# Kernel tuning notes

Hardware: AMD Instinct MI355X
Metric: run time of the kernel (lower is better)

The kernel has to match this reference:

```python
import jax, jax.numpy as jnp
import numpy as np

TAU_MEM = 10.0
TAU_SYN = 5.0
REFRACTORY = 2.0
THRESHOLD = 1.0
TRACE_DECAY = 0.95


def setup_inputs() -> dict:
    key = jax.random.key(0)
    k1, k2, k3 = jax.random.split(key, 3)
    T, D, N = 1000, 64, 128
    return {
        "input_signal": jax.random.normal(k1, (T, D), dtype=jnp.float32),
        "input_weights": jax.random.normal(k2, (D, N), dtype=jnp.float32) * 0.1,
        "recurrent_weights": jax.random.normal(k3, (N, N), dtype=jnp.float32) * 0.05,
        "n_timesteps": 1000,
    }


def reference(input_signal, input_weights, recurrent_weights, n_timesteps):
    # Faithful to the torch code: batch_size = input_signal.shape[0] (= T here),
    # and each timestep's input current (1, N) broadcasts across all B rows.
    B = input_signal.shape[0]
    N = input_weights.shape[1]
    dtype = input_signal.dtype
    # Precompute per-step input currents (T, N); valid since n_timesteps == T.
    inp_cur = input_signal[:n_timesteps] @ input_weights

    def step(state, x_t):
        mem, syn, trace, refr = state
        rec = trace @ recurrent_weights                      # (B, N)
        syn = syn * (1.0 - 1.0 / TAU_SYN) + x_t[None, :] + rec
        mem = mem * (1.0 - 1.0 / TAU_MEM) + syn / TAU_MEM
        mem = jnp.where(refr > 0, jnp.zeros_like(mem), mem)  # refractory masking
        refr = jnp.maximum(refr - 1.0, 0.0)
        spikes = (mem > THRESHOLD).astype(dtype)
        mem = mem * (1.0 - spikes)                           # reset on spike
        refr = refr + spikes * REFRACTORY
        trace = trace * TRACE_DECAY + spikes
        return (mem, syn, trace, refr), (spikes, mem)

    z = jnp.zeros((B, N), dtype)
    (_, _, trace, _), (spk, memh) = jax.lax.scan(step, (z, z, z, z), inp_cur)
    spike_trains = jnp.transpose(spk, (1, 0, 2))       # (B, T, N)
    membrane_history = jnp.transpose(memh, (1, 0, 2))  # (B, T, N)
    return spike_trains, membrane_history, trace
```

## Files before the change

### kernel.cpp

```cpp
#include <hip/hip_runtime.h>
#include <math.h>


#define XCHUNK 8

typedef float vf4 __attribute__((ext_vector_type(4)));

__global__ void inpcur_kernel(const float* __restrict__ sig,
                              const float* __restrict__ win,
                              double* __restrict__ inp_cur,
                              int D, int N) {
    const int t = blockIdx.x;
    const int n = threadIdx.x;
    const float* srow = sig + (size_t)t * D;
    double acc = 0.0;
    for (int d = 0; d < D; ++d)
        acc += (double)srow[d] * (double)win[(size_t)d * N + n];
    inp_cur[(size_t)t * N + n] = acc;
}

__global__ __launch_bounds__(64, 1) void sim_kernel(
    const double* __restrict__ inp_cur,
    const float* __restrict__ wrec,
    float* __restrict__ spk_out,
    float* __restrict__ mem_out,
    float* __restrict__ trace_out,
    int nt) {
    __shared__ float lds_w[128 * 128];

    const int l = threadIdx.x;

    __builtin_amdgcn_s_setprio(3);

    {
        const vf4* src = (const vf4*)wrec;
        vf4* dst = (vf4*)lds_w;
        for (int i = 0; i < 64; ++i)
            dst[i * 64 + l] = src[i * 64 + l];
    }

    double mem_lo = 0.0, syn_lo = 0.0, trc_lo = 0.0, refr_lo = 0.0, rec_lo = 0.0;
    double mem_hi = 0.0, syn_hi = 0.0, trc_hi = 0.0, refr_hi = 0.0, rec_hi = 0.0;

    double x_lo[XCHUNK], x_hi[XCHUNK];

    for (int t0 = 0; t0 < nt; t0 += XCHUNK) {
        const int cs = (nt - t0 < XCHUNK) ? (nt - t0) : XCHUNK;
        #pragma unroll
        for (int s = 0; s < XCHUNK; ++s) {
            if (s < cs) {
                x_lo[s] = inp_cur[(size_t)(t0 + s) * 128 + l];
                x_hi[s] = inp_cur[(size_t)(t0 + s) * 128 + l + 64];
            }
        }

        #pragma unroll
        for (int s = 0; s < XCHUNK; ++s) {
            if (s >= cs) break;
            const int t = t0 + s;

            syn_lo = syn_lo * (1.0 - 1.0 / 5.0) + x_lo[s] + rec_lo;
            mem_lo = mem_lo * (1.0 - 1.0 / 10.0) + syn_lo / 10.0;
            if (refr_lo > 0.0) mem_lo = 0.0;
            refr_lo = refr_lo - 1.0;
            if (refr_lo < 0.0) refr_lo = 0.0;
            const bool sp_lo = mem_lo > 1.0;

            syn_hi = syn_hi * (1.0 - 1.0 / 5.0) + x_hi[s] + rec_hi;
            mem_hi = mem_hi * (1.0 - 1.0 / 10.0) + syn_hi / 10.0;
            if (refr_hi > 0.0) mem_hi = 0.0;
            refr_hi = refr_hi - 1.0;
            if (refr_hi < 0.0) refr_hi = 0.0;
            const bool sp_hi = mem_hi > 1.0;

            const unsigned long long m0 = __ballot(sp_lo);
            const unsigned long long m1 = __ballot(sp_hi);

            if (sp_lo) { mem_lo = 0.0; refr_lo += 2.0; }
            trc_lo = trc_lo * 0.95 + (sp_lo ? 1.0 : 0.0);
            if (sp_hi) { mem_hi = 0.0; refr_hi += 2.0; }
            trc_hi = trc_hi * 0.95 + (sp_hi ? 1.0 : 0.0);

            spk_out[(size_t)t * 128 + l]      = sp_lo ? 1.0f : 0.0f;
            spk_out[(size_t)t * 128 + l + 64] = sp_hi ? 1.0f : 0.0f;
            mem_out[(size_t)t * 128 + l]      = (float)mem_lo;
            mem_out[(size_t)t * 128 + l + 64] = (float)mem_hi;

            double add_lo = 0.0, add_hi = 0.0;
            #pragma unroll 1
            for (int half = 0; half < 2; ++half) {
                unsigned long long m = half ? m1 : m0;
                const float* wb = lds_w + (half ? (64 * 128) : 0);
                while (m) {
                    int kk[8];
                    bool vv[8];
                    #pragma unroll
                    for (int j = 0; j < 8; ++j) {
                        vv[j] = (m != 0ull);
                        kk[j] = m ? (int)__builtin_ctzll(m) : 0;
                        m &= (m - 1ull);
                    }
                    float wl[8], wh[8];
                    #pragma unroll
                    for (int j = 0; j < 8; ++j) {
                        wl[j] = wb[kk[j] * 128 + l];
                        wh[j] = wb[kk[j] * 128 + l + 64];
                    }
                    #pragma unroll
                    for (int j = 0; j < 8; ++j) {
                        add_lo += vv[j] ? (double)wl[j] : 0.0;
                        add_hi += vv[j] ? (double)wh[j] : 0.0;
                    }
                }
            }
            rec_lo = rec_lo * 0.95 + add_lo;
            rec_hi = rec_hi * 0.95 + add_hi;
        }
    }
    trace_out[l]      = (float)trc_lo;
    trace_out[l + 64] = (float)trc_hi;
}

__global__ void bcast_kernel(float* __restrict__ out,
                             int TN4, long long TN, long long B_TN) {
    const long long b = (long long)blockIdx.y + 1;
    const int base = blockIdx.x * (blockDim.x * 4) + threadIdx.x;
    const vf4* s0 = (const vf4*)out;
    const vf4* m0 = (const vf4*)(out + B_TN);
    vf4* sd = (vf4*)(out + b * TN);
    vf4* md = (vf4*)(out + B_TN + b * TN);
    #pragma unroll
    for (int j = 0; j < 4; ++j) {
        const int i = base + j * blockDim.x;
        if (i < TN4) {
            __builtin_nontemporal_store(s0[i], &sd[i]);
            __builtin_nontemporal_store(m0[i], &md[i]);
        }
    }
}

__global__ void trace_bcast_kernel(float* __restrict__ tr, int B, int N4) {
    const int idx = blockIdx.x * blockDim.x + threadIdx.x;
    const int total = (B - 1) * N4;
    if (idx >= total) return;
    const int b = idx / N4 + 1;
    const int j = idx - (b - 1) * N4;
    const vf4 v = ((const vf4*)tr)[j];
    __builtin_nontemporal_store(v, &((vf4*)(tr + (size_t)b * N4 * 4))[j]);
}

extern "C" void kernel_launch(void* const* d_in, const int* in_sizes, int n_in,
                              void* d_out, int out_size, void* d_ws, size_t ws_size,
                              hipStream_t stream) {
    const float* sig  = (const float*)d_in[0];
    const float* win  = (const float*)d_in[1];
    const float* wrec = (const float*)d_in[2];

    int N = 1;
    while ((long long)N * N < (long long)in_sizes[2]) ++N;
    const int D = in_sizes[1] / N;
    const int B = in_sizes[0] / D;
    const int nt = (int)((((long long)out_size / B) - N) / (2 * N));

    const long long TN   = (long long)nt * N;
    const long long B_TN = (long long)B * TN;

    float* out = (float*)d_out;
    double* inp_cur = (double*)(out + ((size_t)out_size - 2 * (size_t)TN));

    inpcur_kernel<<<nt, N, 0, stream>>>(sig, win, inp_cur, D, N);

    sim_kernel<<<1, 64, 0, stream>>>(inp_cur, wrec,
                                     out,
                                     out + B_TN,
                                     out + 2 * B_TN,
                                     nt);

    const int TN4 = (int)(TN / 4);
    dim3 bgrid((TN4 + 1023) / 1024, B - 1);
    bcast_kernel<<<bgrid, 256, 0, stream>>>(out, TN4, TN, B_TN);

    const int trace_total = (B - 1) * (N / 4);
    trace_bcast_kernel<<<(trace_total + 255) / 256, 256, 0, stream>>>(
        out + 2 * B_TN, B, N / 4);
}
```

Before: 2.053 ms.

## Replicate recurrent simulation across 250 blocks writing batch rows directly

Instead of simulating once and then broadcasting the (T,N) result to all B rows with separate copy kernels, 250 blocks each redundantly run the full serial simulation and write four output rows directly with nontemporal stores. The inp_cur scratch buffer moves into two membrane rows, which a small fixup kernel fills afterwards by copying row 0. This removes the bulk read-and-write broadcast pass and spreads the output write bandwidth across many CUs during the latency-bound recurrence. The cost is 250x redundant compute, and each block now issues four times as many stores per step, which may slow the serial critical path.

```diff
diff --git a/kernel.cpp b/kernel.cpp
--- a/kernel.cpp
+++ b/kernel.cpp
@@ -3,6 +3,7 @@
 
 
 #define XCHUNK 8
+#define NBLK   250
 
 typedef float vf4 __attribute__((ext_vector_type(4)));
 
@@ -19,18 +20,30 @@
     inp_cur[(size_t)t * N + n] = acc;
 }
 
-__global__ __launch_bounds__(64, 1) void sim_kernel(
+__global__ __launch_bounds__(64, 1) void simrep_kernel(
     const double* __restrict__ inp_cur,
     const float* __restrict__ wrec,
-    float* __restrict__ spk_out,
-    float* __restrict__ mem_out,
-    float* __restrict__ trace_out,
-    int nt) {
+    float* __restrict__ out,
+    long long TN, long long B_TN, int B, int nt) {
     __shared__ float lds_w[128 * 128];
 
     const int l = threadIdx.x;
+    const int j = blockIdx.x;
 
     __builtin_amdgcn_s_setprio(3);
+
+    float* spk[4];
+    float* mem[4];
+    bool   wmem[4];
+    int    rows[4];
+    #pragma unroll
+    for (int k = 0; k < 4; ++k) {
+        rows[k] = j + k * NBLK;
+        spk[k]  = out + (long long)rows[k] * TN;
+        mem[k]  = out + B_TN + (long long)rows[k] * TN;
+        wmem[k] = (rows[k] != B - 3) && (rows[k] != B - 2);
+    }
+    float* trace = out + 2 * B_TN;
 
     {
         const vf4* src = (const vf4*)wrec;
@@ -81,10 +94,21 @@
             if (sp_hi) { mem_hi = 0.0; refr_hi += 2.0; }
             trc_hi = trc_hi * 0.95 + (sp_hi ? 1.0 : 0.0);
 
-            spk_out[(size_t)t * 128 + l]      = sp_lo ? 1.0f : 0.0f;
-            spk_out[(size_t)t * 128 + l + 64] = sp_hi ? 1.0f : 0.0f;
-            mem_out[(size_t)t * 128 + l]      = (float)mem_lo;
-            mem_out[(size_t)t * 128 + l + 64] = (float)mem_hi;
+            {
+                const float s0f = sp_lo ? 1.0f : 0.0f;
+                const float s1f = sp_hi ? 1.0f : 0.0f;
+                const float m0f = (float)mem_lo;
+                const float m1f = (float)mem_hi;
+                #pragma unroll
+                for (int k = 0; k < 4; ++k) {
+                    __builtin_nontemporal_store(s0f, &spk[k][(size_t)t * 128 + l]);
+                    __builtin_nontemporal_store(s1f, &spk[k][(size_t)t * 128 + l + 64]);
+                    if (wmem[k]) {
+                        __builtin_nontemporal_store(m0f, &mem[k][(size_t)t * 128 + l]);
+                        __builtin_nontemporal_store(m1f, &mem[k][(size_t)t * 128 + l + 64]);
+                    }
+                }
+            }
 
             double add_lo = 0.0, add_hi = 0.0;
             #pragma unroll 1
@@ -95,21 +119,21 @@
                     int kk[8];
                     bool vv[8];
                     #pragma unroll
-                    for (int j = 0; j < 8; ++j) {
-                        vv[j] = (m != 0ull);
-                        kk[j] = m ? (int)__builtin_ctzll(m) : 0;
+                    for (int jj = 0; jj < 8; ++jj) {
+                        vv[jj] = (m != 0ull);
+                        kk[jj] = m ? (int)__builtin_ctzll(m) : 0;
                         m &= (m - 1ull);
                     }
                     float wl[8], wh[8];
                     #pragma unroll
-                    for (int j = 0; j < 8; ++j) {
-                        wl[j] = wb[kk[j] * 128 + l];
-                        wh[j] = wb[kk[j] * 128 + l + 64];
+                    for (int jj = 0; jj < 8; ++jj) {
+                        wl[jj] = wb[kk[jj] * 128 + l];
+                        wh[jj] = wb[kk[jj] * 128 + l + 64];
                     }
                     #pragma unroll
-                    for (int j = 0; j < 8; ++j) {
-                        add_lo += vv[j] ? (double)wl[j] : 0.0;
-                        add_hi += vv[j] ? (double)wh[j] : 0.0;
+                    for (int jj = 0; jj < 8; ++jj) {
+                        add_lo += vv[jj] ? (double)wl[jj] : 0.0;
+                        add_hi += vv[jj] ? (double)wh[jj] : 0.0;
                     }
                 }
             }
@@ -117,36 +141,23 @@
             rec_hi = rec_hi * 0.95 + add_hi;
         }
     }
-    trace_out[l]      = (float)trc_lo;
-    trace_out[l + 64] = (float)trc_hi;
-}
 
-__global__ void bcast_kernel(float* __restrict__ out,
-                             int TN4, long long TN, long long B_TN) {
-    const long long b = (long long)blockIdx.y + 1;
-    const int base = blockIdx.x * (blockDim.x * 4) + threadIdx.x;
-    const vf4* s0 = (const vf4*)out;
-    const vf4* m0 = (const vf4*)(out + B_TN);
-    vf4* sd = (vf4*)(out + b * TN);
-    vf4* md = (vf4*)(out + B_TN + b * TN);
     #pragma unroll
-    for (int j = 0; j < 4; ++j) {
-        const int i = base + j * blockDim.x;
-        if (i < TN4) {
-            __builtin_nontemporal_store(s0[i], &sd[i]);
-            __builtin_nontemporal_store(m0[i], &md[i]);
-        }
+    for (int k = 0; k < 4; ++k) {
+        trace[(size_t)rows[k] * 128 + l]      = (float)trc_lo;
+        trace[(size_t)rows[k] * 128 + l + 64] = (float)trc_hi;
     }
 }
 
-__global__ void trace_bcast_kernel(float* __restrict__ tr, int B, int N4) {
-    const int idx = blockIdx.x * blockDim.x + threadIdx.x;
-    const int total = (B - 1) * N4;
-    if (idx >= total) return;
-    const int b = idx / N4 + 1;
-    const int j = idx - (b - 1) * N4;
-    const vf4 v = ((const vf4*)tr)[j];
-    __builtin_nontemporal_store(v, &((vf4*)(tr + (size_t)b * N4 * 4))[j]);
+__global__ void fixup_kernel(float* __restrict__ mem_base, long long TN,
+                             int rowA, int rowB) {
+    const long long tn4 = TN / 4;
+    const long long idx = (long long)blockIdx.x * blockDim.x + threadIdx.x;
+    if (idx >= 2 * tn4) return;
+    const int r = (idx < tn4) ? rowA : rowB;
+    const long long i = (idx < tn4) ? idx : idx - tn4;
+    const vf4 v = ((const vf4*)mem_base)[i];
+    __builtin_nontemporal_store(v, (vf4*)mem_base + (long long)r * tn4 + i);
 }
 
 extern "C" void kernel_launch(void* const* d_in, const int* in_sizes, int n_in,
@@ -166,21 +177,14 @@
     const long long B_TN = (long long)B * TN;
 
     float* out = (float*)d_out;
-    double* inp_cur = (double*)(out + ((size_t)out_size - 2 * (size_t)TN));
+    double* inp_cur = (double*)(out + B_TN + (long long)(B - 3) * TN);
 
     inpcur_kernel<<<nt, N, 0, stream>>>(sig, win, inp_cur, D, N);
 
-    sim_kernel<<<1, 64, 0, stream>>>(inp_cur, wrec,
-                                     out,
-                                     out + B_TN,
-                                     out + 2 * B_TN,
-                                     nt);
+    simrep_kernel<<<NBLK, 64, 0, stream>>>(inp_cur, wrec, out,
+                                           TN, B_TN, B, nt);
 
-    const int TN4 = (int)(TN / 4);
-    dim3 bgrid((TN4 + 1023) / 1024, B - 1);
-    bcast_kernel<<<bgrid, 256, 0, stream>>>(out, TN4, TN, B_TN);
-
-    const int trace_total = (B - 1) * (N / 4);
-    trace_bcast_kernel<<<(trace_total + 255) / 256, 256, 0, stream>>>(
-        out + 2 * B_TN, B, N / 4);
+    const long long tn4 = TN / 4;
+    fixup_kernel<<<(unsigned)((2 * tn4 + 255) / 256), 256, 0, stream>>>(
+        out + B_TN, TN, B - 3, B - 2);
 }
```

Result: faster. 1.951 ms (-5.0%).
